# Kernel optimization log

Measured on AMD Instinct MI355X. Metric: run time of the kernel, lower is better.

Reference implementation:

```python
import jax, jax.numpy as jnp
import numpy as np

B, L, C, S, D = 2, 64, 256, 256, 512

def setup_inputs() -> dict:
    key = jax.random.key(0)
    ks = jax.random.split(key, 6)
    scale = 1.0 / np.sqrt(D)
    return {
        "queries": jax.random.normal(ks[0], (B, L, C, D), dtype=jnp.float32),
        "keys": jax.random.normal(ks[1], (B, L, S, D), dtype=jnp.float32),
        "values": jax.random.normal(ks[2], (B, L, S, D), dtype=jnp.float32),
        "Wq": jax.random.normal(ks[3], (D, D), dtype=jnp.float32) * scale,
        "bq": jnp.zeros((D,), dtype=jnp.float32),
        "Wkv": jax.random.normal(ks[4], (D, D), dtype=jnp.float32) * scale,
        "bkv": jnp.zeros((D,), dtype=jnp.float32),
        "Wo": jax.random.normal(ks[5], (D, D), dtype=jnp.float32) * scale,
        "bo": jnp.zeros((D,), dtype=jnp.float32),
    }

def reference(queries, keys, values, Wq, bq, Wkv, bkv, Wo, bo):
    d = queries.shape[-1]
    scale = 1.0 / jnp.sqrt(jnp.asarray(d, queries.dtype))
    # linear projections (torch Linear: x @ W.T + b); kv_projection shared for K and V
    q = queries @ Wq.T + bq            # [B, L, C, D]
    k = keys @ Wkv.T + bkv             # [B, L, S, D]
    v = values @ Wkv.T + bkv           # [B, L, S, D]
    scores = jnp.einsum('blcd,blsd->blcs', q, k)
    attn = jax.nn.softmax(scale * scores, axis=-1)  # dropout is identity in eval
    out = jnp.einsum('blcs,blsd->blcd', attn, v)
    return out @ Wo.T + bo
```

## Files before the change

### kernel.cpp

```cpp
#include <hip/hip_runtime.h>
#include <hip/hip_fp16.h>
#include <stdint.h>


typedef _Float16 f16;
typedef __attribute__((ext_vector_type(8))) _Float16 f16x8;
typedef __attribute__((ext_vector_type(4))) _Float16 f16x4;
typedef __attribute__((ext_vector_type(4))) float f32x4;

#define BK 64

__device__ __forceinline__ void glds16(const void* g, void* l)
{
    __builtin_amdgcn_global_load_lds(
        (const __attribute__((address_space(1))) void*)(uintptr_t)g,
        (__attribute__((address_space(3))) void*)(uint32_t)(uintptr_t)l,
        16, 0, 0);
}

__global__ __launch_bounds__(512)
void proj3(const float* __restrict__ qin, const float* __restrict__ kin,
           const float* __restrict__ vin, const f16* __restrict__ wq,
           const f16* __restrict__ wkv, const float* __restrict__ bq,
           const float* __restrict__ bkv, f16* __restrict__ qh,
           f16* __restrict__ kh, f16* __restrict__ vT)
{
    __shared__ f16 As[128][64];
    __shared__ f16 Bs[128][64];

    const int p     = blockIdx.x;
    const int which = p >> 10;
    const int inner = p & 1023;
    const int xcd   = inner & 7;
    const int slot  = inner >> 3;
    const int m0 = (xcd + 8 * (slot >> 2)) * 128;
    const int n0 = (slot & 3) * 128;

    const float* A    = (which == 0) ? qin : (which == 1) ? kin : vin;
    const f16*   Bt   = (which == 0) ? wq : wkv;
    const float* bias = (which == 0) ? bq : bkv;

    const int tid  = threadIdx.x;
    const int lane = tid & 63;
    const int wave = tid >> 6;
    const int quad = lane >> 4;
    const int l16  = lane & 15;
    const int wr   = wave >> 2;
    const int wc   = wave & 3;

    f32x4 acc[4][2];
    #pragma unroll
    for (int i = 0; i < 4; ++i)
        #pragma unroll
        for (int j = 0; j < 2; ++j)
            acc[i][j] = (f32x4){0.f, 0.f, 0.f, 0.f};

    const int i8 = lane >> 3;
    const int cl = (((lane & 7) - i8) & 7) * 8;

    const int ar = tid >> 2;
    const int ac = (tid & 3) * 16;

    float4 pre[4];
    auto load_a = [&](int k0) {
        const float* s = A + (long)(m0 + ar) * 512 + k0 + ac;
        pre[0] = ((const float4*)s)[0];
        pre[1] = ((const float4*)s)[1];
        pre[2] = ((const float4*)s)[2];
        pre[3] = ((const float4*)s)[3];
    };
    auto store_a = [&]() {
        const int rot = (ar & 7) * 8;
        f16x8 v0, v1;
        v0[0] = (f16)pre[0].x; v0[1] = (f16)pre[0].y;
        v0[2] = (f16)pre[0].z; v0[3] = (f16)pre[0].w;
        v0[4] = (f16)pre[1].x; v0[5] = (f16)pre[1].y;
        v0[6] = (f16)pre[1].z; v0[7] = (f16)pre[1].w;
        v1[0] = (f16)pre[2].x; v1[1] = (f16)pre[2].y;
        v1[2] = (f16)pre[2].z; v1[3] = (f16)pre[2].w;
        v1[4] = (f16)pre[3].x; v1[5] = (f16)pre[3].y;
        v1[6] = (f16)pre[3].z; v1[7] = (f16)pre[3].w;
        *(f16x8*)&As[ar][(ac + rot) & 63]     = v0;
        *(f16x8*)&As[ar][(ac + 8 + rot) & 63] = v1;
    };

    for (int k0 = 0; k0 < 512; k0 += BK) {
        if (k0 == 0) load_a(0);
        if (k0) __syncthreads();
        #pragma unroll
        for (int g = 0; g < 2; ++g) {
            const int R0 = (wave * 2 + g) * 8;
            glds16(Bt + (long)(n0 + R0 + i8) * 512 + k0 + cl, &Bs[R0][0]);
        }
        store_a();
        __syncthreads();
        if (k0 + BK < 512) load_a(k0 + BK);

        #pragma unroll
        for (int ksub = 0; ksub < 2; ++ksub) {
            f16x8 af[4], bf[2];
            #pragma unroll
            for (int i = 0; i < 4; ++i) {
                const int r  = wr * 64 + i * 16 + l16;
                const int pc = ((ksub * 32 + quad * 8) + ((r & 7) * 8)) & 63;
                af[i] = *(const f16x8*)&As[r][pc];
            }
            #pragma unroll
            for (int j = 0; j < 2; ++j) {
                const int r  = wc * 32 + j * 16 + l16;
                const int pc = ((ksub * 32 + quad * 8) + ((r & 7) * 8)) & 63;
                bf[j] = *(const f16x8*)&Bs[r][pc];
            }
            #pragma unroll
            for (int i = 0; i < 4; ++i)
                #pragma unroll
                for (int j = 0; j < 2; ++j)
                    acc[i][j] = __builtin_amdgcn_mfma_f32_16x16x32_f16(
                        af[i], bf[j], acc[i][j], 0, 0, 0);
        }
    }

    f16* qout = (which == 0) ? qh : kh;
    #pragma unroll
    for (int i = 0; i < 4; ++i) {
        #pragma unroll
        for (int j = 0; j < 2; ++j) {
            const int col = n0 + wc * 32 + j * 16 + l16;
            const float bv = bias[col];
            #pragma unroll
            for (int r = 0; r < 4; ++r) {
                const int row = m0 + wr * 64 + i * 16 + quad * 4 + r;
                const float val = acc[i][j][r] + bv;
                if (which == 2)
                    vT[(long)(row >> 8) * 131072 + (long)col * 256 + (row & 255)] = (f16)val;
                else
                    qout[(long)row * 512 + col] = (f16)val;
            }
        }
    }
}

__global__ __launch_bounds__(512)
void gemm_out(const f16* __restrict__ Ah, const f16* __restrict__ Bt,
              const float* __restrict__ bias, float* __restrict__ C)
{
    __shared__ f16 As[128][64];
    __shared__ f16 Bs[128][64];

    const int p    = blockIdx.x;
    const int xcd  = p & 7;
    const int slot = p >> 3;
    const int m0 = (xcd + 8 * (slot >> 2)) * 128;
    const int n0 = (slot & 3) * 128;

    const int tid  = threadIdx.x;
    const int lane = tid & 63;
    const int wave = tid >> 6;
    const int quad = lane >> 4;
    const int l16  = lane & 15;
    const int wr   = wave >> 2;
    const int wc   = wave & 3;

    f32x4 acc[4][2];
    #pragma unroll
    for (int i = 0; i < 4; ++i)
        #pragma unroll
        for (int j = 0; j < 2; ++j)
            acc[i][j] = (f32x4){0.f, 0.f, 0.f, 0.f};

    const int i8 = lane >> 3;
    const int cl = (((lane & 7) - i8) & 7) * 8;

    for (int k0 = 0; k0 < 512; k0 += BK) {
        if (k0) __syncthreads();
        #pragma unroll
        for (int g = 0; g < 2; ++g) {
            const int R0 = (wave * 2 + g) * 8;
            glds16(Ah + (long)(m0 + R0 + i8) * 512 + k0 + cl, &As[R0][0]);
            glds16(Bt + (long)(n0 + R0 + i8) * 512 + k0 + cl, &Bs[R0][0]);
        }
        __syncthreads();

        #pragma unroll
        for (int ksub = 0; ksub < 2; ++ksub) {
            f16x8 af[4], bf[2];
            #pragma unroll
            for (int i = 0; i < 4; ++i) {
                const int r  = wr * 64 + i * 16 + l16;
                const int pc = ((ksub * 32 + quad * 8) + ((r & 7) * 8)) & 63;
                af[i] = *(const f16x8*)&As[r][pc];
            }
            #pragma unroll
            for (int j = 0; j < 2; ++j) {
                const int r  = wc * 32 + j * 16 + l16;
                const int pc = ((ksub * 32 + quad * 8) + ((r & 7) * 8)) & 63;
                bf[j] = *(const f16x8*)&Bs[r][pc];
            }
            #pragma unroll
            for (int i = 0; i < 4; ++i)
                #pragma unroll
                for (int j = 0; j < 2; ++j)
                    acc[i][j] = __builtin_amdgcn_mfma_f32_16x16x32_f16(
                        af[i], bf[j], acc[i][j], 0, 0, 0);
        }
    }

    #pragma unroll
    for (int i = 0; i < 4; ++i) {
        #pragma unroll
        for (int j = 0; j < 2; ++j) {
            const int col = n0 + wc * 32 + j * 16 + l16;
            const float bv = bias[col];
            #pragma unroll
            for (int r = 0; r < 4; ++r) {
                const int row = m0 + wr * 64 + i * 16 + quad * 4 + r;
                C[(long)row * 512 + col] = acc[i][j][r] + bv;
            }
        }
    }
}

__global__ __launch_bounds__(512)
void attn_fused(const f16* __restrict__ q, const f16* __restrict__ k,
                const f16* __restrict__ vT, f16* __restrict__ O)
{
    __shared__ __align__(16) f16 bufA[128 * 256];
    __shared__ __align__(16) f16 Vs[4][128][64];
    __shared__ float red[2][128][4];

    f16 (*As)[BK]  = (f16(*)[BK])bufA;
    f16 (*Bs)[BK]  = (f16(*)[BK])(bufA + 128 * 64);
    f16 (*Ps)[256] = (f16(*)[256])bufA;

    const int p    = blockIdx.x;
    const int xcd  = p & 7;
    const int slot = p >> 3;
    const int z    = xcd + 8 * (slot >> 1);
    const int m0   = (slot & 1) * 128;

    const int tid  = threadIdx.x;
    const int lane = tid & 63;
    const int wave = tid >> 6;
    const int quad = lane >> 4;
    const int l16  = lane & 15;
    const int wr   = wave >> 2;
    const int wc   = wave & 3;

    const f16* Aq = q  + (long)z * 131072 + (long)m0 * 512;
    const f16* Bk = k  + (long)z * 131072;
    const f16* Vt = vT + (long)z * 131072;

    f32x4 acc[4][4];
    #pragma unroll
    for (int i = 0; i < 4; ++i)
        #pragma unroll
        for (int j = 0; j < 4; ++j)
            acc[i][j] = (f32x4){0.f, 0.f, 0.f, 0.f};

    const int i8 = lane >> 3;
    const int cl = (((lane & 7) - i8) & 7) * 8;

    for (int k0 = 0; k0 < 512; k0 += BK) {
        if (k0) __syncthreads();
        #pragma unroll
        for (int g = 0; g < 2; ++g) {
            const int R0 = (wave * 2 + g) * 8;
            glds16(Aq + (long)(R0 + i8) * 512 + k0 + cl, &As[R0][0]);
        }
        #pragma unroll
        for (int g = 0; g < 4; ++g) {
            const int R0 = (wave * 4 + g) * 8;
            glds16(Bk + (long)(R0 + i8) * 512 + k0 + cl, &Bs[R0][0]);
        }
        __syncthreads();

        #pragma unroll
        for (int ksub = 0; ksub < 2; ++ksub) {
            f16x8 af[4], bf[4];
            #pragma unroll
            for (int i = 0; i < 4; ++i) {
                const int r  = wr * 64 + i * 16 + l16;
                const int pc = ((ksub * 32 + quad * 8) + ((r & 7) * 8)) & 63;
                af[i] = *(const f16x8*)&As[r][pc];
            }
            #pragma unroll
            for (int j = 0; j < 4; ++j) {
                const int r  = wc * 64 + j * 16 + l16;
                const int pc = ((ksub * 32 + quad * 8) + ((r & 7) * 8)) & 63;
                bf[j] = *(const f16x8*)&Bs[r][pc];
            }
            #pragma unroll
            for (int i = 0; i < 4; ++i)
                #pragma unroll
                for (int j = 0; j < 4; ++j)
                    acc[i][j] = __builtin_amdgcn_mfma_f32_16x16x32_f16(
                        af[i], bf[j], acc[i][j], 0, 0, 0);
        }
    }

    const float scale = 0.044194173824159216f;
    float st[4][4];
    #pragma unroll
    for (int i = 0; i < 4; ++i)
        #pragma unroll
        for (int r = 0; r < 4; ++r) {
            float m = acc[i][0][r];
            #pragma unroll
            for (int j = 1; j < 4; ++j) m = fmaxf(m, acc[i][j][r]);
            st[i][r] = m;
        }
    #pragma unroll
    for (int off = 1; off < 16; off <<= 1)
        #pragma unroll
        for (int i = 0; i < 4; ++i)
            #pragma unroll
            for (int r = 0; r < 4; ++r)
                st[i][r] = fmaxf(st[i][r], __shfl_xor(st[i][r], off, 64));
    if (l16 == 0)
        #pragma unroll
        for (int i = 0; i < 4; ++i)
            #pragma unroll
            for (int r = 0; r < 4; ++r)
                red[0][wr * 64 + i * 16 + quad * 4 + r][wc] = st[i][r];
    __syncthreads();

    #pragma unroll
    for (int i = 0; i < 4; ++i)
        #pragma unroll
        for (int r = 0; r < 4; ++r) {
            const int row = wr * 64 + i * 16 + quad * 4 + r;
            const float m = fmaxf(fmaxf(red[0][row][0], red[0][row][1]),
                                  fmaxf(red[0][row][2], red[0][row][3]));
            float s = 0.f;
            #pragma unroll
            for (int j = 0; j < 4; ++j) {
                const float e = __expf(scale * (acc[i][j][r] - m));
                s += e;
                const int col = wc * 64 + j * 16 + l16;
                Ps[row][(col & 192) + (((col & 63) + ((row & 7) * 8)) & 63)] = (f16)e;
            }
            st[i][r] = s;
        }
    #pragma unroll
    for (int off = 1; off < 16; off <<= 1)
        #pragma unroll
        for (int i = 0; i < 4; ++i)
            #pragma unroll
            for (int r = 0; r < 4; ++r)
                st[i][r] += __shfl_xor(st[i][r], off, 64);
    if (l16 == 0)
        #pragma unroll
        for (int i = 0; i < 4; ++i)
            #pragma unroll
            for (int r = 0; r < 4; ++r)
                red[1][wr * 64 + i * 16 + quad * 4 + r][wc] = st[i][r];
    __syncthreads();

    if (tid < 128) {
        const float s = red[1][tid][0] + red[1][tid][1] +
                        red[1][tid][2] + red[1][tid][3];
        red[0][tid][0] = 1.0f / s;
    }

    for (int nc = 0; nc < 4; ++nc) {
        const int n0c = nc * 128;
        __syncthreads();
        #pragma unroll
        for (int kb = 0; kb < 4; ++kb)
            #pragma unroll
            for (int g = 0; g < 2; ++g) {
                const int R0 = (wave * 2 + g) * 8;
                glds16(Vt + (long)(n0c + R0 + i8) * 256 + kb * 64 + cl,
                       &Vs[kb][R0][0]);
            }
        __syncthreads();

        f32x4 acc2[4][2];
        #pragma unroll
        for (int i = 0; i < 4; ++i)
            #pragma unroll
            for (int j = 0; j < 2; ++j)
                acc2[i][j] = (f32x4){0.f, 0.f, 0.f, 0.f};

        #pragma unroll
        for (int kb = 0; kb < 4; ++kb)
            #pragma unroll
            for (int ksub = 0; ksub < 2; ++ksub) {
                f16x8 af[4], bf[2];
                #pragma unroll
                for (int i = 0; i < 4; ++i) {
                    const int r  = wr * 64 + i * 16 + l16;
                    const int pc = kb * 64 +
                        (((ksub * 32 + quad * 8) + ((r & 7) * 8)) & 63);
                    af[i] = *(const f16x8*)&Ps[r][pc];
                }
                #pragma unroll
                for (int j = 0; j < 2; ++j) {
                    const int rv = wc * 32 + j * 16 + l16;
                    const int pc = ((ksub * 32 + quad * 8) + ((rv & 7) * 8)) & 63;
                    bf[j] = *(const f16x8*)&Vs[kb][rv][pc];
                }
                #pragma unroll
                for (int i = 0; i < 4; ++i)
                    #pragma unroll
                    for (int j = 0; j < 2; ++j)
                        acc2[i][j] = __builtin_amdgcn_mfma_f32_16x16x32_f16(
                            af[i], bf[j], acc2[i][j], 0, 0, 0);
            }

        #pragma unroll
        for (int i = 0; i < 4; ++i)
            #pragma unroll
            for (int j = 0; j < 2; ++j) {
                const int col = n0c + wc * 32 + j * 16 + l16;
                #pragma unroll
                for (int rr = 0; rr < 4; ++rr) {
                    const int row = wr * 64 + i * 16 + quad * 4 + rr;
                    const float inv = red[0][row][0];
                    O[(long)z * 131072 + (long)(m0 + row) * 512 + col] =
                        (f16)(acc2[i][j][rr] * inv);
                }
            }
    }
}

__global__ __launch_bounds__(256)
void cvt3(const float* __restrict__ a, const float* __restrict__ b,
          const float* __restrict__ c, f16* __restrict__ oa,
          f16* __restrict__ ob, f16* __restrict__ oc)
{
    const int w = blockIdx.x >> 8;
    const int t = ((blockIdx.x & 255) * 256 + threadIdx.x) * 4;
    const float* src = (w == 0) ? a : (w == 1) ? b : c;
    f16* dst = (w == 0) ? oa : (w == 1) ? ob : oc;
    const float4 v = *(const float4*)(src + t);
    f16x4 o;
    o[0] = (f16)v.x; o[1] = (f16)v.y; o[2] = (f16)v.z; o[3] = (f16)v.w;
    *(f16x4*)(dst + t) = o;
}

extern "C" void kernel_launch(void* const* d_in, const int* in_sizes, int n_in,
                              void* d_out, int out_size, void* d_ws, size_t ws_size,
                              hipStream_t stream)
{
    const float* queries = (const float*)d_in[0];
    const float* keys    = (const float*)d_in[1];
    const float* values  = (const float*)d_in[2];
    const float* Wq      = (const float*)d_in[3];
    const float* bq      = (const float*)d_in[4];
    const float* Wkv     = (const float*)d_in[5];
    const float* bkv     = (const float*)d_in[6];
    const float* Wo      = (const float*)d_in[7];
    const float* bo      = (const float*)d_in[8];
    float* out = (float*)d_out;

    f16* ws  = (f16*)d_ws;
    f16* wq  = ws;
    f16* wkv = ws + 262144;
    f16* wo  = ws + 524288;
    f16* qh  = ws + 786432;
    f16* kh  = qh + 16777216;
    f16* vT  = kh + 16777216;
    f16* ao  = qh;

    cvt3<<<768, 256, 0, stream>>>(Wq, Wkv, Wo, wq, wkv, wo);

    proj3<<<3072, dim3(512), 0, stream>>>(
        queries, keys, values, wq, wkv, bq, bkv, qh, kh, vT);

    attn_fused<<<256, 512, 0, stream>>>(qh, kh, vT, ao);

    gemm_out<<<1024, dim3(512), 0, stream>>>(ao, wo, bo, out);
}
```

Before: 391.7 us.

## Load fp32 A tiles directly to LDS and use 4-wave 64x64 warp tiles

In the projection kernel, the fp32 activation tile is now copied straight into shared memory with async global-to-LDS loads using a rotated swizzle. It is converted to fp16 at fragment-read time, replacing the register prefetch, convert and store path. Both GEMM kernels move from 8 waves with 64x32 warp tiles to 4 waves with 64x64 warp tiles, which gives more MFMA per fragment load but doubles accumulator registers per thread. The fp32 LDS buffer doubles A-tile shared memory, and the conversion now happens once per consumer wave rather than once per tile.

```diff
diff --git a/kernel.cpp b/kernel.cpp
--- a/kernel.cpp
+++ b/kernel.cpp
@@ -18,15 +18,15 @@
         16, 0, 0);
 }
 
-__global__ __launch_bounds__(512)
+__global__ __launch_bounds__(256)
 void proj3(const float* __restrict__ qin, const float* __restrict__ kin,
            const float* __restrict__ vin, const f16* __restrict__ wq,
            const f16* __restrict__ wkv, const float* __restrict__ bq,
            const float* __restrict__ bkv, f16* __restrict__ qh,
            f16* __restrict__ kh, f16* __restrict__ vT)
 {
-    __shared__ f16 As[128][64];
-    __shared__ f16 Bs[128][64];
+    __shared__ __align__(16) float Asf[128][64];
+    __shared__ __align__(16) f16  Bs[128][64];
 
     const int p     = blockIdx.x;
     const int which = p >> 10;
@@ -45,76 +45,65 @@
     const int wave = tid >> 6;
     const int quad = lane >> 4;
     const int l16  = lane & 15;
-    const int wr   = wave >> 2;
-    const int wc   = wave & 3;
-
-    f32x4 acc[4][2];
+    const int wr   = wave >> 1;
+    const int wc   = wave & 1;
+
+    f32x4 acc[4][4];
     #pragma unroll
     for (int i = 0; i < 4; ++i)
         #pragma unroll
-        for (int j = 0; j < 2; ++j)
+        for (int j = 0; j < 4; ++j)
             acc[i][j] = (f32x4){0.f, 0.f, 0.f, 0.f};
 
     const int i8 = lane >> 3;
     const int cl = (((lane & 7) - i8) & 7) * 8;
 
-    const int ar = tid >> 2;
-    const int ac = (tid & 3) * 16;
-
-    float4 pre[4];
-    auto load_a = [&](int k0) {
-        const float* s = A + (long)(m0 + ar) * 512 + k0 + ac;
-        pre[0] = ((const float4*)s)[0];
-        pre[1] = ((const float4*)s)[1];
-        pre[2] = ((const float4*)s)[2];
-        pre[3] = ((const float4*)s)[3];
-    };
-    auto store_a = [&]() {
-        const int rot = (ar & 7) * 8;
-        f16x8 v0, v1;
-        v0[0] = (f16)pre[0].x; v0[1] = (f16)pre[0].y;
-        v0[2] = (f16)pre[0].z; v0[3] = (f16)pre[0].w;
-        v0[4] = (f16)pre[1].x; v0[5] = (f16)pre[1].y;
-        v0[6] = (f16)pre[1].z; v0[7] = (f16)pre[1].w;
-        v1[0] = (f16)pre[2].x; v1[1] = (f16)pre[2].y;
-        v1[2] = (f16)pre[2].z; v1[3] = (f16)pre[2].w;
-        v1[4] = (f16)pre[3].x; v1[5] = (f16)pre[3].y;
-        v1[6] = (f16)pre[3].z; v1[7] = (f16)pre[3].w;
-        *(f16x8*)&As[ar][(ac + rot) & 63]     = v0;
-        *(f16x8*)&As[ar][(ac + 8 + rot) & 63] = v1;
-    };
+    const int ar4 = lane >> 4;
 
     for (int k0 = 0; k0 < 512; k0 += BK) {
-        if (k0 == 0) load_a(0);
         if (k0) __syncthreads();
         #pragma unroll
-        for (int g = 0; g < 2; ++g) {
-            const int R0 = (wave * 2 + g) * 8;
+        for (int g = 0; g < 8; ++g) {
+            const int R0  = (wave * 8 + g) * 4;
+            const int row = R0 + ar4;
+            const int gcol = ((lane & 15) - (row & 7)) & 15;
+            glds16(A + (long)(m0 + row) * 512 + k0 + gcol * 4, &Asf[R0][0]);
+        }
+        #pragma unroll
+        for (int g = 0; g < 4; ++g) {
+            const int R0 = (wave * 4 + g) * 8;
             glds16(Bt + (long)(n0 + R0 + i8) * 512 + k0 + cl, &Bs[R0][0]);
         }
-        store_a();
         __syncthreads();
-        if (k0 + BK < 512) load_a(k0 + BK);
 
         #pragma unroll
         for (int ksub = 0; ksub < 2; ++ksub) {
-            f16x8 af[4], bf[2];
+            f16x8 af[4], bf[4];
             #pragma unroll
             for (int i = 0; i < 4; ++i) {
                 const int r  = wr * 64 + i * 16 + l16;
-                const int pc = ((ksub * 32 + quad * 8) + ((r & 7) * 8)) & 63;
-                af[i] = *(const f16x8*)&As[r][pc];
-            }
-            #pragma unroll
-            for (int j = 0; j < 2; ++j) {
-                const int r  = wc * 32 + j * 16 + l16;
+                const int g0 = ksub * 8 + quad * 2;
+                const int ga = (g0 + (r & 7)) & 15;
+                const int gb = (g0 + 1 + (r & 7)) & 15;
+                const f32x4 a0 = *(const f32x4*)&Asf[r][ga * 4];
+                const f32x4 a1 = *(const f32x4*)&Asf[r][gb * 4];
+                f16x8 v;
+                v[0] = (f16)a0[0]; v[1] = (f16)a0[1];
+                v[2] = (f16)a0[2]; v[3] = (f16)a0[3];
+                v[4] = (f16)a1[0]; v[5] = (f16)a1[1];
+                v[6] = (f16)a1[2]; v[7] = (f16)a1[3];
+                af[i] = v;
+            }
+            #pragma unroll
+            for (int j = 0; j < 4; ++j) {
+                const int r  = wc * 64 + j * 16 + l16;
                 const int pc = ((ksub * 32 + quad * 8) + ((r & 7) * 8)) & 63;
                 bf[j] = *(const f16x8*)&Bs[r][pc];
             }
             #pragma unroll
             for (int i = 0; i < 4; ++i)
                 #pragma unroll
-                for (int j = 0; j < 2; ++j)
+                for (int j = 0; j < 4; ++j)
                     acc[i][j] = __builtin_amdgcn_mfma_f32_16x16x32_f16(
                         af[i], bf[j], acc[i][j], 0, 0, 0);
         }
@@ -124,8 +113,8 @@
     #pragma unroll
     for (int i = 0; i < 4; ++i) {
         #pragma unroll
-        for (int j = 0; j < 2; ++j) {
-            const int col = n0 + wc * 32 + j * 16 + l16;
+        for (int j = 0; j < 4; ++j) {
+            const int col = n0 + wc * 64 + j * 16 + l16;
             const float bv = bias[col];
             #pragma unroll
             for (int r = 0; r < 4; ++r) {
@@ -140,7 +129,7 @@
     }
 }
 
-__global__ __launch_bounds__(512)
+__global__ __launch_bounds__(256)
 void gemm_out(const f16* __restrict__ Ah, const f16* __restrict__ Bt,
               const float* __restrict__ bias, float* __restrict__ C)
 {
@@ -158,14 +147,14 @@
     const int wave = tid >> 6;
     const int quad = lane >> 4;
     const int l16  = lane & 15;
-    const int wr   = wave >> 2;
-    const int wc   = wave & 3;
-
-    f32x4 acc[4][2];
+    const int wr   = wave >> 1;
+    const int wc   = wave & 1;
+
+    f32x4 acc[4][4];
     #pragma unroll
     for (int i = 0; i < 4; ++i)
         #pragma unroll
-        for (int j = 0; j < 2; ++j)
+        for (int j = 0; j < 4; ++j)
             acc[i][j] = (f32x4){0.f, 0.f, 0.f, 0.f};
 
     const int i8 = lane >> 3;
@@ -174,8 +163,8 @@
     for (int k0 = 0; k0 < 512; k0 += BK) {
         if (k0) __syncthreads();
         #pragma unroll
-        for (int g = 0; g < 2; ++g) {
-            const int R0 = (wave * 2 + g) * 8;
+        for (int j = 0; j < 4; ++j) {
+            const int R0 = (wave * 4 + j) * 8;
             glds16(Ah + (long)(m0 + R0 + i8) * 512 + k0 + cl, &As[R0][0]);
             glds16(Bt + (long)(n0 + R0 + i8) * 512 + k0 + cl, &Bs[R0][0]);
         }
@@ -183,7 +172,7 @@
 
         #pragma unroll
         for (int ksub = 0; ksub < 2; ++ksub) {
-            f16x8 af[4], bf[2];
+            f16x8 af[4], bf[4];
             #pragma unroll
             for (int i = 0; i < 4; ++i) {
                 const int r  = wr * 64 + i * 16 + l16;
@@ -191,15 +180,15 @@
                 af[i] = *(const f16x8*)&As[r][pc];
             }
             #pragma unroll
-            for (int j = 0; j < 2; ++j) {
-                const int r  = wc * 32 + j * 16 + l16;
+            for (int j = 0; j < 4; ++j) {
+                const int r  = wc * 64 + j * 16 + l16;
                 const int pc = ((ksub * 32 + quad * 8) + ((r & 7) * 8)) & 63;
                 bf[j] = *(const f16x8*)&Bs[r][pc];
             }
             #pragma unroll
             for (int i = 0; i < 4; ++i)
                 #pragma unroll
-                for (int j = 0; j < 2; ++j)
+                for (int j = 0; j < 4; ++j)
                     acc[i][j] = __builtin_amdgcn_mfma_f32_16x16x32_f16(
                         af[i], bf[j], acc[i][j], 0, 0, 0);
         }
@@ -208,8 +197,8 @@
     #pragma unroll
     for (int i = 0; i < 4; ++i) {
         #pragma unroll
-        for (int j = 0; j < 2; ++j) {
-            const int col = n0 + wc * 32 + j * 16 + l16;
+        for (int j = 0; j < 4; ++j) {
+            const int col = n0 + wc * 64 + j * 16 + l16;
             const float bv = bias[col];
             #pragma unroll
             for (int r = 0; r < 4; ++r) {
@@ -465,10 +454,10 @@
 
     cvt3<<<768, 256, 0, stream>>>(Wq, Wkv, Wo, wq, wkv, wo);
 
-    proj3<<<3072, dim3(512), 0, stream>>>(
+    proj3<<<3072, dim3(256), 0, stream>>>(
         queries, keys, values, wq, wkv, bq, bkv, qh, kh, vT);
 
     attn_fused<<<256, 512, 0, stream>>>(qh, kh, vT, ao);
 
-    gemm_out<<<1024, dim3(512), 0, stream>>>(ao, wo, bo, out);
-}
+    gemm_out<<<1024, dim3(256), 0, stream>>>(ao, wo, bo, out);
+}
```

New measurement: 360.0 us. -8.1%, faster.
